# Performance work log

Hardware: AMD Instinct MI355X
Metric: run time of the kernel (lower is better)

The kernel has to match this reference:

```python
import jax, jax.numpy as jnp
import numpy as np

B, L, C, H, DK, MAXR = 2, 2048, 256, 8, 32, 7
NEG = jnp.float32(-2**32 + 1)


def _rel_tab(L, maxR):
    # |i-j| with log2 bucketing beyond maxR, clipped to [0, 2*maxR]
    i = jnp.arange(L)
    d = jnp.abs(i[:, None] - i[None, :]).astype(jnp.float32)
    d = jnp.where(d > maxR, maxR + jnp.log2(jnp.maximum(d - maxR, 1.0)), d)
    return jnp.clip(d, 0, 2 * maxR).astype(jnp.int32)  # [L, L]


def setup_inputs() -> dict:
    key = jax.random.key(0)
    ks = jax.random.split(key, 14)
    s = 0.02
    return {
        "qx": jax.random.normal(ks[0], (B, L, C), jnp.float32),
        "kx": jax.random.normal(ks[1], (B, L, C), jnp.float32),
        "vx": jax.random.normal(ks[2], (B, L, C), jnp.float32),
        "preScores": jax.random.normal(ks[3], (B, H, L, L), jnp.float32),
        "maskPAD": jnp.ones((B, L, L), jnp.int32),
        "WQ_w": jax.random.normal(ks[4], (C, H * DK), jnp.float32) * s,
        "WQ_b": jnp.zeros((H * DK,), jnp.float32),
        "WK_w": jax.random.normal(ks[5], (C, H * DK), jnp.float32) * s,
        "WK_b": jnp.zeros((H * DK,), jnp.float32),
        "WV_w": jax.random.normal(ks[6], (C, H * DK), jnp.float32) * s,
        "WV_b": jnp.zeros((H * DK,), jnp.float32),
        "WO_w": jax.random.normal(ks[7], (H * DK, C), jnp.float32) * s,
        "WO_b": jnp.zeros((C,), jnp.float32),
        "embK": jax.random.normal(ks[8], (2 * MAXR + 1, H), jnp.float32),
        "embB": jax.random.normal(ks[9], (2 * MAXR + 1, H), jnp.float32),
    }


def reference(qx, kx, vx, preScores, maskPAD,
              WQ_w, WQ_b, WK_w, WK_b, WV_w, WV_b, WO_w, WO_b, embK, embB):
    q = (qx @ WQ_w + WQ_b).reshape(B, L, H, DK)
    k = (kx @ WK_w + WK_b).reshape(B, L, H, DK)
    v = (vx @ WV_w + WV_b).reshape(B, L, H, DK)
    scores = jnp.einsum('blhd,bmhd->bhlm', q, k) / jnp.float32(np.sqrt(DK))
    tab = _rel_tab(L, MAXR)                       # [L, L] int32
    kb = jnp.transpose(embK[tab], (2, 0, 1))[None]  # [1, H, L, L]
    bb = jnp.transpose(embB[tab], (2, 0, 1))[None]
    scores = scores * kb + bb + preScores
    scores = jnp.where(maskPAD[:, None, :, :] == 0, NEG, scores)
    alpha = jax.nn.softmax(scores, axis=3)        # dropout = identity (eval)
    z = jnp.einsum('bhlm,bmhd->blhd', alpha, v).reshape(B, L, H * DK)
    z = z @ WO_w + WO_b
    return (z, scores)
```

## Files before the change

kernel.cpp:

```cpp
#include <hip/hip_runtime.h>
#include <hip/hip_bf16.h>
#include <math.h>

typedef __bf16 bf16;
typedef __bf16 bf16x8 __attribute__((ext_vector_type(8)));
typedef __bf16 bf16x4 __attribute__((ext_vector_type(4)));
typedef float  f32x4  __attribute__((ext_vector_type(4)));
typedef int    i32x4  __attribute__((ext_vector_type(4)));

#define NB 2
#define NL 2048
#define NC 256
#define NH 8
#define NDK 32
#define JSPLIT 4
#define JCHUNK (NL / JSPLIT)
#define JTILES (JCHUNK / 64)
#define SCALE 0.17677669529663687f
#define NEGV  -4294967296.0f

#define PIN() __builtin_amdgcn_sched_barrier(0)
#define LDSFENCE() do { \
    asm volatile("s_waitcnt lgkmcnt(0)" ::: "memory"); \
    __builtin_amdgcn_sched_barrier(0); } while (0)

__global__ __launch_bounds__(256) void proj_kernel(
    const float* __restrict__ qx, const float* __restrict__ kx, const float* __restrict__ vx,
    const float* __restrict__ Wq, const float* __restrict__ bq,
    const float* __restrict__ Wk, const float* __restrict__ bk,
    const float* __restrict__ Wv, const float* __restrict__ bv,
    bf16* __restrict__ qo, bf16* __restrict__ ko, bf16* __restrict__ vto)
{
    const int mode = blockIdx.z;
    const float* X    = (mode == 0) ? qx : (mode == 1) ? kx : vx;
    const float* W    = (mode == 0) ? Wq : (mode == 1) ? Wk : Wv;
    const float* bias = (mode == 0) ? bq : (mode == 1) ? bk : bv;

    __shared__ float As[64][33];
    __shared__ float Bs[32][65];

    const int tid = threadIdx.x;
    const int tx = tid & 15, ty = tid >> 4;
    const int m0 = blockIdx.x * 64, n0 = blockIdx.y * 64;

    float acc[4][4] = {{0.f}};

    for (int k0 = 0; k0 < NC; k0 += 32) {
        const int ar = tid >> 2, ac = (tid & 3) << 3;
        const float4 a0 = *(const float4*)(X + (size_t)(m0 + ar) * NC + k0 + ac);
        const float4 a1 = *(const float4*)(X + (size_t)(m0 + ar) * NC + k0 + ac + 4);
        const int br = tid >> 3, bc = (tid & 7) << 3;
        const float4 b0 = *(const float4*)(W + (size_t)(k0 + br) * NC + n0 + bc);
        const float4 b1 = *(const float4*)(W + (size_t)(k0 + br) * NC + n0 + bc + 4);
        __syncthreads();
        As[ar][ac+0]=a0.x; As[ar][ac+1]=a0.y; As[ar][ac+2]=a0.z; As[ar][ac+3]=a0.w;
        As[ar][ac+4]=a1.x; As[ar][ac+5]=a1.y; As[ar][ac+6]=a1.z; As[ar][ac+7]=a1.w;
        Bs[br][bc+0]=b0.x; Bs[br][bc+1]=b0.y; Bs[br][bc+2]=b0.z; Bs[br][bc+3]=b0.w;
        Bs[br][bc+4]=b1.x; Bs[br][bc+5]=b1.y; Bs[br][bc+6]=b1.z; Bs[br][bc+7]=b1.w;
        __syncthreads();
        #pragma unroll
        for (int kk = 0; kk < 32; ++kk) {
            float av[4], bw[4];
            #pragma unroll
            for (int r = 0; r < 4; ++r) av[r] = As[ty*4+r][kk];
            #pragma unroll
            for (int c = 0; c < 4; ++c) bw[c] = Bs[kk][tx*4+c];
            #pragma unroll
            for (int r = 0; r < 4; ++r)
                #pragma unroll
                for (int c = 0; c < 4; ++c)
                    acc[r][c] = fmaf(av[r], bw[c], acc[r][c]);
        }
    }

    #pragma unroll
    for (int r = 0; r < 4; ++r) {
        const int row = m0 + ty*4 + r;
        const int bb_ = row >> 11, ll = row & (NL - 1);
        #pragma unroll
        for (int c = 0; c < 4; ++c) {
            const int col = n0 + tx*4 + c;
            const float v = acc[r][c] + bias[col];
            const int hh = col >> 5, d = col & 31;
            if (mode == 0)
                qo[(((size_t)bb_*NH + hh)*NL + ll)*NDK + d] = (bf16)v;
            else if (mode == 1)
                ko[(((size_t)bb_*NH + hh)*NL + ll)*NDK + d] = (bf16)v;
            else
                vto[(((size_t)bb_*NH + hh)*NDK + d)*NL + ll] = (bf16)v;
        }
    }
}

__global__ __launch_bounds__(256) void out_gemm_kernel(
    const float* __restrict__ zp, const float* __restrict__ lbuf,
    const float* __restrict__ W, const float* __restrict__ bias,
    float* __restrict__ out)
{
    __shared__ float As[32][33];
    __shared__ float Bs[32][65];

    const int tid = threadIdx.x;
    const int tx = tid & 15, ty = tid >> 4;
    const int m0 = blockIdx.x * 32, n0 = blockIdx.y * 64;

    float acc[2][4] = {{0.f}};

    for (int k0 = 0; k0 < NC; k0 += 32) {
        const int hh = k0 >> 5;
        const int ar = tid >> 3, ac = (tid & 7) << 2;
        const int m = m0 + ar;
        const int bq_ = m >> 11, i = m & (NL - 1);
        const int bh = bq_ * NH + hh;
        f32x4 a = {0.f, 0.f, 0.f, 0.f};
        float L = 0.f;
        #pragma unroll
        for (int js = 0; js < JSPLIT; ++js) {
            const size_t base = ((size_t)(bh * JSPLIT + js) * NL + i);
            a += *(const f32x4*)(zp + base * NDK + ac);
            L += lbuf[base];
        }
        const float rL = 1.0f / L;

        const int br = tid >> 3, bc = (tid & 7) << 3;
        const float4 b0 = *(const float4*)(W + (size_t)(k0 + br) * NC + n0 + bc);
        const float4 b1 = *(const float4*)(W + (size_t)(k0 + br) * NC + n0 + bc + 4);
        __syncthreads();
        As[ar][ac+0]=a[0]*rL; As[ar][ac+1]=a[1]*rL; As[ar][ac+2]=a[2]*rL; As[ar][ac+3]=a[3]*rL;
        Bs[br][bc+0]=b0.x; Bs[br][bc+1]=b0.y; Bs[br][bc+2]=b0.z; Bs[br][bc+3]=b0.w;
        Bs[br][bc+4]=b1.x; Bs[br][bc+5]=b1.y; Bs[br][bc+6]=b1.z; Bs[br][bc+7]=b1.w;
        __syncthreads();
        #pragma unroll
        for (int kk = 0; kk < 32; ++kk) {
            float av[2], bw[4];
            av[0] = As[ty*2+0][kk];
            av[1] = As[ty*2+1][kk];
            #pragma unroll
            for (int c = 0; c < 4; ++c) bw[c] = Bs[kk][tx*4+c];
            #pragma unroll
            for (int r = 0; r < 2; ++r)
                #pragma unroll
                for (int c = 0; c < 4; ++c)
                    acc[r][c] = fmaf(av[r], bw[c], acc[r][c]);
        }
    }

    #pragma unroll
    for (int r = 0; r < 2; ++r) {
        const int row = m0 + ty*2 + r;
        #pragma unroll
        for (int c = 0; c < 4; ++c) {
            const int col = n0 + tx*4 + c;
            out[(size_t)row * NC + col] = acc[r][c] + bias[col];
        }
    }
}

__global__ __launch_bounds__(64) void attn_kernel(
    const bf16* __restrict__ q, const bf16* __restrict__ k, const bf16* __restrict__ vt,
    const float* __restrict__ preScores, const int* __restrict__ maskPAD,
    const float* __restrict__ embK, const float* __restrict__ embB,
    float* __restrict__ scores_out, float* __restrict__ zp, float* __restrict__ lbuf)
{
    const int h  = blockIdx.x & (NH - 1);
    const int i0 = (blockIdx.x >> 3) << 4;
    const int js = blockIdx.y;
    const int b  = blockIdx.z;
    const int lane = threadIdx.x & 63;
    const int l15 = lane & 15, g = lane >> 4;

    __shared__ __align__(16) bf16 Ps[16][72];
    __shared__ float2 tab[16];

    if (lane < 15) tab[lane] = make_float2(embK[lane * NH + h], embB[lane * NH + h]);
    LDSFENCE();

    const size_t bh = (size_t)b * NH + h;
    const int i_row = i0 + l15;
    const bf16x8 bQ = *(const bf16x8*)(q + (bh * NL + i_row) * NDK + g * 8);

    const int jc0 = js * JCHUNK;
    const bf16*  kptr  = k  + (bh * NL + jc0 + l15) * NDK + (g << 3);
    const bf16*  vptr  = vt + (bh * NDK + l15) * NL + jc0 + (g << 3);
    const bf16*  vptr2 = vptr + 16 * NL;
    const float* pptr  = preScores + (bh * NL + i_row) * (size_t)NL + jc0 + (g << 2);
    const int*   mptr  = maskPAD + ((size_t)b * NL + i_row) * (size_t)NL + jc0 + (g << 2);
    float* scoreRow = scores_out + (bh * NL + i_row) * (size_t)NL;

    uint4 kbuf[4], vbuf[4]; f32x4 pbuf[4]; i32x4 mbuf[4];

    #pragma unroll
    for (int tj = 0; tj < 4; ++tj)
        kbuf[tj] = *(const uint4*)(kptr + (size_t)tj * 16 * NDK);
    #pragma unroll
    for (int tj = 0; tj < 4; ++tj)
        pbuf[tj] = __builtin_nontemporal_load((const f32x4*)(pptr + (tj << 4)));
    #pragma unroll
    for (int tj = 0; tj < 4; ++tj)
        mbuf[tj] = *(const i32x4*)(mptr + (tj << 4));
    vbuf[0] = *(const uint4*)(vptr);
    vbuf[1] = *(const uint4*)(vptr2);
    vbuf[2] = *(const uint4*)(vptr + 32);
    vbuf[3] = *(const uint4*)(vptr2 + 32);
    PIN();

    f32x4 oF0 = {0.f, 0.f, 0.f, 0.f};
    f32x4 oF1 = {0.f, 0.f, 0.f, 0.f};
    const f32x4 zf = {0.f, 0.f, 0.f, 0.f};
    float l_lane = 0.f;

    #pragma unroll
    for (int jt = 0; jt < JTILES; ++jt) {
        const int j0 = jc0 + (jt << 6);
        const bool more = (jt + 1 < JTILES);

        f32x4 sf[4];
        #pragma unroll
        for (int tj = 0; tj < 4; ++tj)
            sf[tj] = __builtin_amdgcn_mfma_f32_16x16x32_bf16(
                __builtin_bit_cast(bf16x8, kbuf[tj]), bQ, zf, 0, 0, 0);

        if (more) {
            #pragma unroll
            for (int tj = 0; tj < 4; ++tj)
                kbuf[tj] = *(const uint4*)(kptr + (size_t)(jt + 1) * 64 * NDK
                                                + (size_t)tj * 16 * NDK);
            PIN();
        }

        #pragma unroll
        for (int tj = 0; tj < 4; ++tj) {
            const int jb = j0 + (tj << 4) + (g << 2);
            f32x4 out4; bf16x4 pk;
            #pragma unroll
            for (int r = 0; r < 4; ++r) {
                const int j = jb + r;
                int dd = i_row - j; dd = dd < 0 ? -dd : dd;
                int idx = dd;
                if (dd > 7) {
                    idx = 38 - __clz(dd - 7);
                    idx = idx > 14 ? 14 : idx;
                }
                const float2 kb2 = tab[idx];
                float sv = sf[tj][r] * SCALE;
                sv = sv * kb2.x + kb2.y + pbuf[tj][r];
                if (mbuf[tj][r] == 0) sv = NEGV;
                out4[r] = sv;
                const float e = __expf(sv);
                l_lane += e;
                pk[r] = (bf16)e;
            }
            *(f32x4*)(scoreRow + jb) = out4;
            *(bf16x4*)&Ps[l15][(tj << 4) | (g << 2)] = pk;
        }

        if (more) {
            #pragma unroll
            for (int tj = 0; tj < 4; ++tj)
                pbuf[tj] = __builtin_nontemporal_load(
                    (const f32x4*)(pptr + ((jt + 1) << 6) + (tj << 4)));
            #pragma unroll
            for (int tj = 0; tj < 4; ++tj)
                mbuf[tj] = *(const i32x4*)(mptr + ((jt + 1) << 6) + (tj << 4));
            PIN();
        }

        LDSFENCE();

        #pragma unroll
        for (int cc = 0; cc < 2; ++cc) {
            const bf16x8 aP = *(const bf16x8*)&Ps[l15][cc * 32 + g * 8];
            oF0 = __builtin_amdgcn_mfma_f32_16x16x32_bf16(
                aP, __builtin_bit_cast(bf16x8, vbuf[cc * 2 + 0]), oF0, 0, 0, 0);
            oF1 = __builtin_amdgcn_mfma_f32_16x16x32_bf16(
                aP, __builtin_bit_cast(bf16x8, vbuf[cc * 2 + 1]), oF1, 0, 0, 0);
        }

        if (more) {
            vbuf[0] = *(const uint4*)(vptr + ((jt + 1) << 6));
            vbuf[1] = *(const uint4*)(vptr2 + ((jt + 1) << 6));
            vbuf[2] = *(const uint4*)(vptr + ((jt + 1) << 6) + 32);
            vbuf[3] = *(const uint4*)(vptr2 + ((jt + 1) << 6) + 32);
            PIN();
        }
    }

    float lsum = l_lane;
    lsum += __shfl_xor(lsum, 16, 64);
    lsum += __shfl_xor(lsum, 32, 64);

    #pragma unroll
    for (int r = 0; r < 4; ++r) {
        const int i = i0 + (g << 2) + r;
        float* zr = zp + ((bh * JSPLIT + js) * (size_t)NL + i) * NDK;
        zr[l15]      = oF0[r];
        zr[16 + l15] = oF1[r];
    }
    if (g == 0)
        lbuf[(bh * JSPLIT + js) * (size_t)NL + i_row] = lsum;
}

extern "C" void kernel_launch(void* const* d_in, const int* in_sizes, int n_in,
                              void* d_out, int out_size, void* d_ws, size_t ws_size,
                              hipStream_t stream) {
    (void)in_sizes; (void)n_in; (void)out_size; (void)ws_size;

    const float* qx        = (const float*)d_in[0];
    const float* kx        = (const float*)d_in[1];
    const float* vx        = (const float*)d_in[2];
    const float* preScores = (const float*)d_in[3];
    const int*   maskPAD   = (const int*)  d_in[4];
    const float* WQ_w      = (const float*)d_in[5];
    const float* WQ_b      = (const float*)d_in[6];
    const float* WK_w      = (const float*)d_in[7];
    const float* WK_b      = (const float*)d_in[8];
    const float* WV_w      = (const float*)d_in[9];
    const float* WV_b      = (const float*)d_in[10];
    const float* WO_w      = (const float*)d_in[11];
    const float* WO_b      = (const float*)d_in[12];
    const float* embK      = (const float*)d_in[13];
    const float* embB      = (const float*)d_in[14];

    char* ws = (char*)d_ws;
    bf16*  qb   = (bf16*)(ws);
    bf16*  kb   = (bf16*)(ws + (2u << 20));
    bf16*  vtb  = (bf16*)(ws + (4u << 20));
    float* zpb  = (float*)(ws + (6u << 20));
    float* lbuf = (float*)(ws + (22u << 20));

    float* z_out      = (float*)d_out;
    float* scores_out = (float*)d_out + (size_t)NB * NL * NC;

    proj_kernel<<<dim3(64, 4, 3), 256, 0, stream>>>(
        qx, kx, vx, WQ_w, WQ_b, WK_w, WK_b, WV_w, WV_b, qb, kb, vtb);

    attn_kernel<<<dim3((NL / 16) * NH, JSPLIT, NB), 64, 0, stream>>>(
        qb, kb, vtb, preScores, maskPAD, embK, embB, scores_out, zpb, lbuf);

    out_gemm_kernel<<<dim3(NB * NL / 32, 4), 256, 0, stream>>>(zpb, lbuf, WO_w, WO_b, z_out);
}
```

Before: 247.9 us.

## Stage preScores/mask through LDS with coalesced row loads and remap blocks for XCD locality

The attention kernel now loads preScores and maskPAD as full 1KB row segments per wave (lane-contiguous), applies the mask while staging into an LDS tile, and finishes the score computation in LDS. The finished scores are then written back with the same coalesced row-wise stores. The grid is flattened into 1D and block IDs are swizzled so consecutive blocks on an XCD share batch/head/j-chunk. The register double-buffering of K, V, preScores and mask is dropped, along with the sched barriers, so K and V are now loaded just in time. This risks exposing load latency, and the 16.6KB LDS tile may reduce occupancy.

```diff
diff --git a/kernel.cpp b/kernel.cpp
--- a/kernel.cpp
+++ b/kernel.cpp
@@ -15,14 +15,8 @@
 #define NDK 32
 #define JSPLIT 4
 #define JCHUNK (NL / JSPLIT)
-#define JTILES (JCHUNK / 64)
 #define SCALE 0.17677669529663687f
 #define NEGV  -4294967296.0f
-
-#define PIN() __builtin_amdgcn_sched_barrier(0)
-#define LDSFENCE() do { \
-    asm volatile("s_waitcnt lgkmcnt(0)" ::: "memory"); \
-    __builtin_amdgcn_sched_barrier(0); } while (0)
 
 __global__ __launch_bounds__(256) void proj_kernel(
     const float* __restrict__ qx, const float* __restrict__ kx, const float* __restrict__ vx,
@@ -162,126 +156,106 @@
     const float* __restrict__ embK, const float* __restrict__ embB,
     float* __restrict__ scores_out, float* __restrict__ zp, float* __restrict__ lbuf)
 {
-    const int h  = blockIdx.x & (NH - 1);
-    const int i0 = (blockIdx.x >> 3) << 4;
-    const int js = blockIdx.y;
-    const int b  = blockIdx.z;
+    const int lbid = blockIdx.x;
+    const int wid  = (lbid & 7) * 1024 + (lbid >> 3);
+    const int i0   = (wid & 127) << 4;
+    const int h    = (wid >> 7) & 7;
+    const int js   = (wid >> 10) & 3;
+    const int b    = wid >> 12;
+
     const int lane = threadIdx.x & 63;
     const int l15 = lane & 15, g = lane >> 4;
 
+    __shared__ __align__(16) float sc[16][260];
     __shared__ __align__(16) bf16 Ps[16][72];
     __shared__ float2 tab[16];
 
     if (lane < 15) tab[lane] = make_float2(embK[lane * NH + h], embB[lane * NH + h]);
-    LDSFENCE();
+    asm volatile("s_waitcnt lgkmcnt(0)" ::: "memory");
 
     const size_t bh = (size_t)b * NH + h;
     const int i_row = i0 + l15;
     const bf16x8 bQ = *(const bf16x8*)(q + (bh * NL + i_row) * NDK + g * 8);
 
     const int jc0 = js * JCHUNK;
-    const bf16*  kptr  = k  + (bh * NL + jc0 + l15) * NDK + (g << 3);
-    const bf16*  vptr  = vt + (bh * NDK + l15) * NL + jc0 + (g << 3);
-    const bf16*  vptr2 = vptr + 16 * NL;
-    const float* pptr  = preScores + (bh * NL + i_row) * (size_t)NL + jc0 + (g << 2);
-    const int*   mptr  = maskPAD + ((size_t)b * NL + i_row) * (size_t)NL + jc0 + (g << 2);
-    float* scoreRow = scores_out + (bh * NL + i_row) * (size_t)NL;
-
-    uint4 kbuf[4], vbuf[4]; f32x4 pbuf[4]; i32x4 mbuf[4];
-
-    #pragma unroll
-    for (int tj = 0; tj < 4; ++tj)
-        kbuf[tj] = *(const uint4*)(kptr + (size_t)tj * 16 * NDK);
-    #pragma unroll
-    for (int tj = 0; tj < 4; ++tj)
-        pbuf[tj] = __builtin_nontemporal_load((const f32x4*)(pptr + (tj << 4)));
-    #pragma unroll
-    for (int tj = 0; tj < 4; ++tj)
-        mbuf[tj] = *(const i32x4*)(mptr + (tj << 4));
-    vbuf[0] = *(const uint4*)(vptr);
-    vbuf[1] = *(const uint4*)(vptr2);
-    vbuf[2] = *(const uint4*)(vptr + 32);
-    vbuf[3] = *(const uint4*)(vptr2 + 32);
-    PIN();
+    const bf16* kptr = k  + (bh * NL + l15) * NDK + (g << 3);
+    const bf16* vptr = vt + (bh * NDK + l15) * NL + (g << 3);
+
+    const float* preBase  = preScores + (bh * NL + i0) * (size_t)NL + 4 * lane;
+    const int*   maskBase = maskPAD + ((size_t)b * NL + i0) * (size_t)NL + 4 * lane;
+    float*       scoBase  = scores_out + (bh * NL + i0) * (size_t)NL + 4 * lane;
 
     f32x4 oF0 = {0.f, 0.f, 0.f, 0.f};
     f32x4 oF1 = {0.f, 0.f, 0.f, 0.f};
     const f32x4 zf = {0.f, 0.f, 0.f, 0.f};
     float l_lane = 0.f;
 
-    #pragma unroll
-    for (int jt = 0; jt < JTILES; ++jt) {
-        const int j0 = jc0 + (jt << 6);
-        const bool more = (jt + 1 < JTILES);
-
-        f32x4 sf[4];
-        #pragma unroll
-        for (int tj = 0; tj < 4; ++tj)
-            sf[tj] = __builtin_amdgcn_mfma_f32_16x16x32_bf16(
-                __builtin_bit_cast(bf16x8, kbuf[tj]), bQ, zf, 0, 0, 0);
-
-        if (more) {
-            #pragma unroll
-            for (int tj = 0; tj < 4; ++tj)
-                kbuf[tj] = *(const uint4*)(kptr + (size_t)(jt + 1) * 64 * NDK
-                                                + (size_t)tj * 16 * NDK);
-            PIN();
-        }
-
-        #pragma unroll
-        for (int tj = 0; tj < 4; ++tj) {
-            const int jb = j0 + (tj << 4) + (g << 2);
-            f32x4 out4; bf16x4 pk;
-            #pragma unroll
-            for (int r = 0; r < 4; ++r) {
-                const int j = jb + r;
-                int dd = i_row - j; dd = dd < 0 ? -dd : dd;
-                int idx = dd;
-                if (dd > 7) {
-                    idx = 38 - __clz(dd - 7);
-                    idx = idx > 14 ? 14 : idx;
+    for (int st = 0; st < JCHUNK / 256; ++st) {
+        const int jsup = jc0 + st * 256;
+
+        #pragma unroll
+        for (int r = 0; r < 16; ++r) {
+            const f32x4 p4 = __builtin_nontemporal_load(
+                (const f32x4*)(preBase + (size_t)r * NL + jsup));
+            const i32x4 m4 = *(const i32x4*)(maskBase + (size_t)r * NL + jsup);
+            f32x4 pe;
+            #pragma unroll
+            for (int c = 0; c < 4; ++c)
+                pe[c] = m4[c] ? p4[c] : NEGV;
+            *(f32x4*)&sc[r][4 * lane] = pe;
+        }
+
+        #pragma unroll
+        for (int jt = 0; jt < 4; ++jt) {
+            const int j0 = jsup + jt * 64;
+
+            f32x4 sf[4];
+            #pragma unroll
+            for (int tj = 0; tj < 4; ++tj) {
+                const bf16x8 aK = *(const bf16x8*)(kptr + (size_t)(j0 + tj * 16) * NDK);
+                sf[tj] = __builtin_amdgcn_mfma_f32_16x16x32_bf16(aK, bQ, zf, 0, 0, 0);
+            }
+
+            #pragma unroll
+            for (int tj = 0; tj < 4; ++tj) {
+                const int jb = jt * 64 + (tj << 4) + (g << 2);
+                const f32x4 pe = *(const f32x4*)&sc[l15][jb];
+                f32x4 out4; bf16x4 pk;
+                #pragma unroll
+                for (int r = 0; r < 4; ++r) {
+                    const int j = jsup + jb + r;
+                    int dd = i_row - j; dd = dd < 0 ? -dd : dd;
+                    int idx = dd;
+                    if (dd > 7) {
+                        idx = 38 - __clz(dd - 7);
+                        idx = idx > 14 ? 14 : idx;
+                    }
+                    const float2 kb2 = tab[idx];
+                    float sv = sf[tj][r] * SCALE;
+                    sv = sv * kb2.x + kb2.y + pe[r];
+                    out4[r] = sv;
+                    const float e = __expf(sv);
+                    l_lane += e;
+                    pk[r] = (bf16)e;
                 }
-                const float2 kb2 = tab[idx];
-                float sv = sf[tj][r] * SCALE;
-                sv = sv * kb2.x + kb2.y + pbuf[tj][r];
-                if (mbuf[tj][r] == 0) sv = NEGV;
-                out4[r] = sv;
-                const float e = __expf(sv);
-                l_lane += e;
-                pk[r] = (bf16)e;
+                *(f32x4*)&sc[l15][jb] = out4;
+                *(bf16x4*)&Ps[l15][(tj << 4) | (g << 2)] = pk;
             }
-            *(f32x4*)(scoreRow + jb) = out4;
-            *(bf16x4*)&Ps[l15][(tj << 4) | (g << 2)] = pk;
-        }
-
-        if (more) {
-            #pragma unroll
-            for (int tj = 0; tj < 4; ++tj)
-                pbuf[tj] = __builtin_nontemporal_load(
-                    (const f32x4*)(pptr + ((jt + 1) << 6) + (tj << 4)));
-            #pragma unroll
-            for (int tj = 0; tj < 4; ++tj)
-                mbuf[tj] = *(const i32x4*)(mptr + ((jt + 1) << 6) + (tj << 4));
-            PIN();
-        }
-
-        LDSFENCE();
-
-        #pragma unroll
-        for (int cc = 0; cc < 2; ++cc) {
-            const bf16x8 aP = *(const bf16x8*)&Ps[l15][cc * 32 + g * 8];
-            oF0 = __builtin_amdgcn_mfma_f32_16x16x32_bf16(
-                aP, __builtin_bit_cast(bf16x8, vbuf[cc * 2 + 0]), oF0, 0, 0, 0);
-            oF1 = __builtin_amdgcn_mfma_f32_16x16x32_bf16(
-                aP, __builtin_bit_cast(bf16x8, vbuf[cc * 2 + 1]), oF1, 0, 0, 0);
-        }
-
-        if (more) {
-            vbuf[0] = *(const uint4*)(vptr + ((jt + 1) << 6));
-            vbuf[1] = *(const uint4*)(vptr2 + ((jt + 1) << 6));
-            vbuf[2] = *(const uint4*)(vptr + ((jt + 1) << 6) + 32);
-            vbuf[3] = *(const uint4*)(vptr2 + ((jt + 1) << 6) + 32);
-            PIN();
+
+            #pragma unroll
+            for (int cc = 0; cc < 2; ++cc) {
+                const bf16x8 aP  = *(const bf16x8*)&Ps[l15][cc * 32 + g * 8];
+                const bf16x8 bV0 = *(const bf16x8*)(vptr + j0 + cc * 32);
+                const bf16x8 bV1 = *(const bf16x8*)(vptr + 16 * NL + j0 + cc * 32);
+                oF0 = __builtin_amdgcn_mfma_f32_16x16x32_bf16(aP, bV0, oF0, 0, 0, 0);
+                oF1 = __builtin_amdgcn_mfma_f32_16x16x32_bf16(aP, bV1, oF1, 0, 0, 0);
+            }
+        }
+
+        #pragma unroll
+        for (int r = 0; r < 16; ++r) {
+            const f32x4 v = *(const f32x4*)&sc[r][4 * lane];
+            *(f32x4*)(scoBase + (size_t)r * NL + jsup) = v;
         }
     }
 
@@ -334,7 +308,7 @@
     proj_kernel<<<dim3(64, 4, 3), 256, 0, stream>>>(
         qx, kx, vx, WQ_w, WQ_b, WK_w, WK_b, WV_w, WV_b, qb, kb, vtb);
 
-    attn_kernel<<<dim3((NL / 16) * NH, JSPLIT, NB), 64, 0, stream>>>(
+    attn_kernel<<<dim3((NL / 16) * NH * JSPLIT * NB), 64, 0, stream>>>(
         qb, kb, vtb, preScores, maskPAD, embK, embB, scores_out, zpb, lbuf);
 
     out_gemm_kernel<<<dim3(NB * NL / 32, 4), 256, 0, stream>>>(zpb, lbuf, WO_w, WO_b, z_out);
```

Measured after the change: 254.2 us. +2.5%, slower.
